# Kernel optimization log

Measured on AMD Instinct MI355X. Metric: run time of the kernel, lower is better.

## Reference

```python
import jax, jax.numpy as jnp
import numpy as np

N_NODES = 10000
N_EDGES = 160000
IN_FEATS = 512
HEADS = 8
OUT_FEATS = 64
NEG_SLOPE = 0.2


def setup_inputs() -> dict:
    key = jax.random.key(0)
    k_feat, k_w, k_al, k_ar, k_src, k_dst = jax.random.split(key, 6)
    feat = jax.random.normal(k_feat, (N_NODES, IN_FEATS), dtype=jnp.float32)
    # fc weight stored as [in_feats, heads*out_feats] (x @ W == Linear without bias)
    W = jax.random.normal(k_w, (IN_FEATS, HEADS * OUT_FEATS), dtype=jnp.float32) * 0.05
    attn_l = jax.random.normal(k_al, (HEADS, OUT_FEATS), dtype=jnp.float32) * 0.1
    attn_r = jax.random.normal(k_ar, (HEADS, OUT_FEATS), dtype=jnp.float32) * 0.1
    bias = jnp.zeros((HEADS * OUT_FEATS,), dtype=jnp.float32)
    src = jax.random.randint(k_src, (N_EDGES,), 0, N_NODES, dtype=jnp.int32)
    dst = jax.random.randint(k_dst, (N_EDGES,), 0, N_NODES, dtype=jnp.int32)
    return {"feat": feat, "W": W, "attn_l": attn_l, "attn_r": attn_r,
            "bias": bias, "src": src, "dst": dst}


def reference(feat, W, attn_l, attn_r, bias, src, dst):
    # 1) project features: [N, H, F]
    h = (feat @ W).reshape(N_NODES, HEADS, OUT_FEATS)
    # 2) per-node attention logits: el_i = a_l . h_i, er_j = a_r . h_j  -> [N, H]
    el = jnp.einsum('nhf,hf->nh', h, attn_l)
    er = jnp.einsum('nhf,hf->nh', h, attn_r)
    # 3) edge scores: u_add_v + LeakyReLU  -> [E, H]
    e = el[src] + er[dst]
    e = jnp.where(e > 0, e, NEG_SLOPE * e)
    # 4) edge softmax over incoming edges of each destination node
    m = jax.ops.segment_max(e, dst, num_segments=N_NODES)  # [N, H]
    a = jnp.exp(e - m[dst])
    s = jax.ops.segment_sum(a, dst, num_segments=N_NODES)  # [N, H]
    a = a / s[dst]
    # 5) weighted scatter-sum aggregation: sum_j a_ij * h_j  -> [N, H, F]
    msg = h[src] * a[:, :, None]                           # [E, H, F]
    rst = jax.ops.segment_sum(msg, dst, num_segments=N_NODES)
    # 6) bias
    rst = rst + bias.reshape(1, HEADS, OUT_FEATS)
    return rst
```

## Files before the change

### kernel.cpp

```cpp
#include <hip/hip_runtime.h>
#include <math.h>

#define N_NODES 10000
#define N_EDGES 160000
#define IN_FEATS 512
#define HEADS 8
#define OUT_FEATS 64
#define HF 512
#define NEG_SLOPE 0.2f
#define M_PAD 10048

typedef float  f32x4  __attribute__((ext_vector_type(4)));
typedef __bf16 bf16x8 __attribute__((ext_vector_type(8)));
typedef short  s16x8  __attribute__((ext_vector_type(8)));

__device__ __forceinline__ unsigned short f2bf_rn(float x) {
    unsigned u = __float_as_uint(x);
    unsigned r = u + 0x7FFFu + ((u >> 16) & 1u);
    return (unsigned short)(r >> 16);
}

__device__ __forceinline__ void gl_lds16(const void* g, void* l) {
    __builtin_amdgcn_global_load_lds((const __attribute__((address_space(1))) void*)g,
                                     (__attribute__((address_space(3))) void*)l, 16, 0, 0);
}

#define SF_BLOCKS 5024
#define PW_BLOCKS 64
#define HIST_BLOCKS 625
__global__ __launch_bounds__(256) void prep_kernel(const float* __restrict__ feat,
                                                   const float* __restrict__ W,
                                                   const int* __restrict__ dst,
                                                   unsigned short* __restrict__ Abf,
                                                   unsigned short* __restrict__ Bt,
                                                   int* __restrict__ counts) {
    __shared__ float tile[64][65];
    const int bid = blockIdx.x;
    const int tid = threadIdx.x;

    if (bid < SF_BLOCKS) {
        const int idx = bid * 256 + tid;
        const int row = idx >> 7;
        const int c4  = idx & 127;
        float4 v = make_float4(0.f, 0.f, 0.f, 0.f);
        if (row < N_NODES)
            v = *reinterpret_cast<const float4*>(feat + (size_t)row * IN_FEATS + c4 * 4);
        ushort4 o;
        o.x = f2bf_rn(v.x);
        o.y = f2bf_rn(v.y);
        o.z = f2bf_rn(v.z);
        o.w = f2bf_rn(v.w);
        *reinterpret_cast<ushort4*>(Abf + (size_t)row * IN_FEATS + c4 * 4) = o;
    } else if (bid < SF_BLOCKS + PW_BLOCKS) {
        const int b2 = bid - SF_BLOCKS;
        const int k0 = (b2 & 7) * 64;
        const int n0 = (b2 >> 3) * 64;
        #pragma unroll
        for (int i = 0; i < 4; ++i) {
            int f = tid + 256 * i;
            int r = f >> 4, c4 = f & 15;
            float4 v = *reinterpret_cast<const float4*>(W + (size_t)(k0 + r) * HF + n0 + c4 * 4);
            tile[r][c4 * 4 + 0] = v.x;
            tile[r][c4 * 4 + 1] = v.y;
            tile[r][c4 * 4 + 2] = v.z;
            tile[r][c4 * 4 + 3] = v.w;
        }
        __syncthreads();
        #pragma unroll
        for (int i = 0; i < 4; ++i) {
            int f = tid + 256 * i;
            int rn = f >> 4, c4 = f & 15;
            ushort4 o;
            o.x = f2bf_rn(tile[c4 * 4 + 0][rn]);
            o.y = f2bf_rn(tile[c4 * 4 + 1][rn]);
            o.z = f2bf_rn(tile[c4 * 4 + 2][rn]);
            o.w = f2bf_rn(tile[c4 * 4 + 3][rn]);
            *reinterpret_cast<ushort4*>(Bt + (size_t)(n0 + rn) * IN_FEATS + k0 + c4 * 4) = o;
        }
    } else {
        const int e = (bid - SF_BLOCKS - PW_BLOCKS) * 256 + tid;
        if (e < N_EDGES) atomicAdd(&counts[dst[e]], 1);
    }
}

#define GTM 64
#define GTN 128
#define GBK 32
__global__ __launch_bounds__(256) void gemm_mfma(const unsigned short* __restrict__ Abf,
                                                 const unsigned short* __restrict__ Bt,
                                                 const float* __restrict__ attn_l,
                                                 const float* __restrict__ attn_r,
                                                 unsigned short* __restrict__ hbf,
                                                 float* __restrict__ el,
                                                 float* __restrict__ er) {
    __shared__ unsigned short sA[2][GTM * GBK];
    __shared__ unsigned short sB[2][GTN * GBK];

    const int tid  = threadIdx.x;
    const int lane = tid & 63;
    const int w    = tid >> 6;
    const int wm   = w >> 1, wn = w & 1;
    const int m16  = lane & 15, quad = lane >> 4;
    const int row0 = blockIdx.y * GTM;
    const int col0 = blockIdx.x * GTN;
    const int hh   = blockIdx.x * 2 + wn;

    const int srow  = lane >> 2;
    const int kperm = ((lane & 3) ^ ((lane >> 4) & 3)) * 8;

    f32x4 acc[2][4] = {};

    auto stage = [&](int nb, int k0) {
        #pragma unroll
        for (int jj = 0; jj < 3; ++jj) {
            const int j = w * 3 + jj;
            if (j < 4) {
                const unsigned short* g = Abf
                    + (size_t)(row0 + j * 16 + srow) * IN_FEATS + k0 + kperm;
                gl_lds16(g, &sA[nb][j * 512]);
            } else {
                const int ch = j - 4;
                const unsigned short* g = Bt
                    + (size_t)(col0 + ch * 16 + srow) * IN_FEATS + k0 + kperm;
                gl_lds16(g, &sB[nb][ch * 512]);
            }
        }
    };

    stage(0, 0);
    int nb = 0;
    const int asw = (quad ^ ((m16 >> 2) & 3)) * 8;

    for (int kt = 0; kt < 16; ++kt) {
        __syncthreads();
        if (kt < 15) stage(nb ^ 1, (kt + 1) * GBK);

        s16x8 fa[2], fb[4];
        #pragma unroll
        for (int mi = 0; mi < 2; ++mi)
            fa[mi] = *reinterpret_cast<const s16x8*>(&sA[nb][(wm * 2 + mi) * 512 + m16 * 32 + asw]);
        #pragma unroll
        for (int ni = 0; ni < 4; ++ni)
            fb[ni] = *reinterpret_cast<const s16x8*>(&sB[nb][(wn * 4 + ni) * 512 + m16 * 32 + asw]);
        #pragma unroll
        for (int mi = 0; mi < 2; ++mi)
            #pragma unroll
            for (int ni = 0; ni < 4; ++ni)
                acc[mi][ni] = __builtin_amdgcn_mfma_f32_16x16x32_bf16(
                    __builtin_bit_cast(bf16x8, fa[mi]), __builtin_bit_cast(bf16x8, fb[ni]),
                    acc[mi][ni], 0, 0, 0);
        nb ^= 1;
    }

    float alw[4], arw[4];
    #pragma unroll
    for (int ni = 0; ni < 4; ++ni) {
        alw[ni] = attn_l[hh * OUT_FEATS + ni * 16 + m16];
        arw[ni] = attn_r[hh * OUT_FEATS + ni * 16 + m16];
    }
    #pragma unroll
    for (int mi = 0; mi < 2; ++mi) {
        #pragma unroll
        for (int r = 0; r < 4; ++r) {
            const int row = row0 + wm * 32 + mi * 16 + quad * 4 + r;
            if (row < N_NODES) {
                float pl = 0.f, pr = 0.f;
                #pragma unroll
                for (int ni = 0; ni < 4; ++ni) {
                    const float v = acc[mi][ni][r];
                    hbf[(size_t)row * HF + hh * OUT_FEATS + ni * 16 + m16] = f2bf_rn(v);
                    pl = fmaf(v, alw[ni], pl);
                    pr = fmaf(v, arw[ni], pr);
                }
                #pragma unroll
                for (int off = 1; off < 16; off <<= 1) {
                    pl += __shfl_xor(pl, off);
                    pr += __shfl_xor(pr, off);
                }
                if (m16 == 0) {
                    el[row * HEADS + hh] = pl;
                    er[row * HEADS + hh] = pr;
                }
            }
        }
    }
}

__global__ __launch_bounds__(1024) void scan_fast(const int* __restrict__ counts,
                                                  int* __restrict__ row_ptr,
                                                  int* __restrict__ cursor) {
    const int t = threadIdx.x;
    const int lane = t & 63, wid = t >> 6;
    for (int i = t; i < N_NODES; i += 1024) cursor[i] = 0;
    int loc[10];
    int tot = 0;
    #pragma unroll
    for (int j = 0; j < 10; ++j) {
        int idx = t * 10 + j;
        int c = (idx < N_NODES) ? counts[idx] : 0;
        loc[j] = tot;
        tot += c;
    }
    int inc = tot;
    #pragma unroll
    for (int off = 1; off < 64; off <<= 1) {
        int nb = __shfl_up(inc, off);
        if (lane >= off) inc += nb;
    }
    __shared__ int wbase[16];
    if (lane == 63) wbase[wid] = inc;
    __syncthreads();
    if (t == 0) {
        int r = 0;
        #pragma unroll
        for (int i = 0; i < 16; ++i) { int x = wbase[i]; wbase[i] = r; r += x; }
    }
    __syncthreads();
    const int base = wbase[wid] + inc - tot;
    #pragma unroll
    for (int j = 0; j < 10; ++j) {
        int idx = t * 10 + j;
        if (idx < N_NODES) row_ptr[idx] = base + loc[j];
    }
    if (t == 1023) row_ptr[N_NODES] = base + tot;
}

__global__ __launch_bounds__(256) void scatter_alpha(const int* __restrict__ src,
                                                     const int* __restrict__ dst,
                                                     const int* __restrict__ row_ptr,
                                                     int* __restrict__ cursor,
                                                     const float* __restrict__ el,
                                                     const float* __restrict__ er,
                                                     int* __restrict__ ssrc,
                                                     float* __restrict__ palpha) {
    const int e = blockIdx.x * 256 + threadIdx.x;
    if (e >= N_EDGES) return;
    const int d  = dst[e];
    const int sn = src[e];
    const int pos = row_ptr[d] + atomicAdd(&cursor[d], 1);
    ssrc[pos] = sn;

    float4 l0 = *reinterpret_cast<const float4*>(el + sn * 8);
    float4 l1 = *reinterpret_cast<const float4*>(el + sn * 8 + 4);
    float4 r0 = *reinterpret_cast<const float4*>(er + d * 8);
    float4 r1 = *reinterpret_cast<const float4*>(er + d * 8 + 4);
    float x[8] = {l0.x + r0.x, l0.y + r0.y, l0.z + r0.z, l0.w + r0.w,
                  l1.x + r1.x, l1.y + r1.y, l1.z + r1.z, l1.w + r1.w};
    float p[8];
    #pragma unroll
    for (int h = 0; h < 8; ++h) {
        float v = x[h] > 0.f ? x[h] : NEG_SLOPE * x[h];
        p[h] = __expf(v);
    }
    *reinterpret_cast<float4*>(palpha + (size_t)pos * 8)     = make_float4(p[0], p[1], p[2], p[3]);
    *reinterpret_cast<float4*>(palpha + (size_t)pos * 8 + 4) = make_float4(p[4], p[5], p[6], p[7]);
}

__global__ __launch_bounds__(256) void aggregate_kernel(const unsigned short* __restrict__ hbf,
                                                        const float* __restrict__ palpha,
                                                        const float* __restrict__ bias,
                                                        const int* __restrict__ row_ptr,
                                                        const int* __restrict__ ssrc,
                                                        float* __restrict__ out) {
    const int n    = (blockIdx.x * 256 + threadIdx.x) >> 6;
    const int lane = threadIdx.x & 63;
    if (n >= N_NODES) return;
    const int head = lane >> 3;
    const int beg = row_ptr[n];
    const int deg = row_ptr[n + 1] - beg;

    float4 b0 = *reinterpret_cast<const float4*>(bias + lane * 8);
    float4 b1 = *reinterpret_cast<const float4*>(bias + lane * 8 + 4);
    float* op = out + (size_t)n * HF + lane * 8;
    if (deg == 0) {
        *reinterpret_cast<float4*>(op)     = b0;
        *reinterpret_cast<float4*>(op + 4) = b1;
        return;
    }

    const int*   __restrict__ sp = ssrc + beg;
    const float* __restrict__ ap = palpha + (size_t)beg * 8 + head;
    const unsigned short* __restrict__ hb = hbf + lane * 8;

    float acc[8] = {};
    float s = 0.f;

    for (int k = 0; k < deg; k += 8) {
        float a[8]; int sx[8];
        #pragma unroll
        for (int j = 0; j < 8; ++j) {
            const int kk = k + j;
            const int kc = (kk < deg) ? kk : 0;
            sx[j] = sp[kc];
            a[j]  = (kk < deg) ? ap[(size_t)kc * 8] : 0.f;
        }
        uint4 u[8];
        #pragma unroll
        for (int j = 0; j < 8; ++j)
            u[j] = *reinterpret_cast<const uint4*>(hb + (size_t)sx[j] * HF);
        #pragma unroll
        for (int j = 0; j < 8; ++j) {
            const unsigned* wp = (const unsigned*)&u[j];
            s += a[j];
            #pragma unroll
            for (int q = 0; q < 4; ++q) {
                acc[2 * q]     = fmaf(a[j], __uint_as_float(wp[q] << 16),         acc[2 * q]);
                acc[2 * q + 1] = fmaf(a[j], __uint_as_float(wp[q] & 0xFFFF0000u), acc[2 * q + 1]);
            }
        }
    }

    const float inv = 1.0f / s;
    float4 o0 = make_float4(acc[0] * inv + b0.x, acc[1] * inv + b0.y,
                            acc[2] * inv + b0.z, acc[3] * inv + b0.w);
    float4 o1 = make_float4(acc[4] * inv + b1.x, acc[5] * inv + b1.y,
                            acc[6] * inv + b1.z, acc[7] * inv + b1.w);
    *reinterpret_cast<float4*>(op)     = o0;
    *reinterpret_cast<float4*>(op + 4) = o1;
}

extern "C" void kernel_launch(void* const* d_in, const int* in_sizes, int n_in,
                              void* d_out, int out_size, void* d_ws, size_t ws_size,
                              hipStream_t stream) {
    const float* feat   = (const float*)d_in[0];
    const float* W      = (const float*)d_in[1];
    const float* attn_l = (const float*)d_in[2];
    const float* attn_r = (const float*)d_in[3];
    const float* bias   = (const float*)d_in[4];
    const int*   src    = (const int*)d_in[5];
    const int*   dst    = (const int*)d_in[6];
    float* out = (float*)d_out;

    char* ws = (char*)d_ws;
    unsigned short* Abf    = (unsigned short*)ws; ws += (size_t)M_PAD * IN_FEATS * 2;
    unsigned short* Bt     = (unsigned short*)ws; ws += (size_t)IN_FEATS * HF * 2;
    unsigned short* hbf    = (unsigned short*)ws; ws += (size_t)N_NODES * HF * 2;
    float*          el_buf = (float*)ws;          ws += (size_t)N_NODES * HEADS * 4;
    float*          er_buf = (float*)ws;          ws += (size_t)N_NODES * HEADS * 4;
    float*          palpha = (float*)ws;          ws += (size_t)N_EDGES * HEADS * 4;
    int*            ssrc   = (int*)ws;            ws += (size_t)N_EDGES * 4;
    int*            counts = (int*)ws;            ws += (size_t)N_NODES * 4;
    int*            cursor = (int*)ws;            ws += (size_t)N_NODES * 4;
    int*            row_ptr= (int*)ws;            ws += (size_t)(N_NODES + 1) * 4;

    hipMemsetAsync(counts, 0, (size_t)N_NODES * 4, stream);

    prep_kernel<<<SF_BLOCKS + PW_BLOCKS + HIST_BLOCKS, 256, 0, stream>>>(
        feat, W, dst, Abf, Bt, counts);

    dim3 ggrid(HF / GTN, M_PAD / GTM);
    gemm_mfma<<<ggrid, 256, 0, stream>>>(Abf, Bt, attn_l, attn_r, hbf, el_buf, er_buf);

    scan_fast<<<1, 1024, 0, stream>>>(counts, row_ptr, cursor);

    scatter_alpha<<<(N_EDGES + 255) / 256, 256, 0, stream>>>(
        src, dst, row_ptr, cursor, el_buf, er_buf, ssrc, palpha);

    aggregate_kernel<<<(N_NODES * 64 + 255) / 256, 256, 0, stream>>>(
        hbf, palpha, bias, row_ptr, ssrc, out);
}
```

Measured before the change: 155.5 us.

## Fold scan into GEMM launch and restructure GEMM to full-K register A tiles

Moves the prefix-scan over in-degree counts into block 0 of the GEMM kernel, which removes one kernel launch. The GEMM is rewritten so each block computes a 64-row by one-head (64-column) tile. It loads the full K=512 slice of B into 64KB of swizzled LDS in a single pass and keeps each wave's A rows in registers for the whole K range, replacing the double-buffered K loop. This drops the per-iteration barriers, but the larger LDS footprint and register use lower occupancy. The scan now runs on 256 threads instead of 1024, which lengthens that block.

```diff
diff --git a/kernel.cpp b/kernel.cpp
--- a/kernel.cpp
+++ b/kernel.cpp
@@ -84,72 +84,95 @@
 }
 
 #define GTM 64
-#define GTN 128
-#define GBK 32
 __global__ __launch_bounds__(256) void gemm_mfma(const unsigned short* __restrict__ Abf,
                                                  const unsigned short* __restrict__ Bt,
                                                  const float* __restrict__ attn_l,
                                                  const float* __restrict__ attn_r,
                                                  unsigned short* __restrict__ hbf,
                                                  float* __restrict__ el,
-                                                 float* __restrict__ er) {
-    __shared__ unsigned short sA[2][GTM * GBK];
-    __shared__ unsigned short sB[2][GTN * GBK];
+                                                 float* __restrict__ er,
+                                                 const int* __restrict__ counts,
+                                                 int* __restrict__ row_ptr,
+                                                 int* __restrict__ cursor) {
+    __shared__ unsigned short sB[64 * 512];
 
     const int tid  = threadIdx.x;
+
+    if (blockIdx.x == 0) {
+        int* wb = (int*)sB;
+        const int lane = tid & 63, wid = tid >> 6;
+        for (int i = tid; i < N_NODES; i += 256) cursor[i] = 0;
+        int loc[40];
+        int tot = 0;
+        #pragma unroll
+        for (int j = 0; j < 40; ++j) {
+            int idx = tid * 40 + j;
+            int c = (idx < N_NODES) ? counts[idx] : 0;
+            loc[j] = tot;
+            tot += c;
+        }
+        int inc = tot;
+        #pragma unroll
+        for (int off = 1; off < 64; off <<= 1) {
+            int nb = __shfl_up(inc, off);
+            if (lane >= off) inc += nb;
+        }
+        if (lane == 63) wb[wid] = inc;
+        __syncthreads();
+        if (tid == 0) {
+            int r = 0;
+            #pragma unroll
+            for (int i = 0; i < 4; ++i) { int x = wb[i]; wb[i] = r; r += x; }
+        }
+        __syncthreads();
+        const int base = wb[wid] + inc - tot;
+        #pragma unroll
+        for (int j = 0; j < 40; ++j) {
+            int idx = tid * 40 + j;
+            if (idx < N_NODES) row_ptr[idx] = base + loc[j];
+        }
+        if (tid == 255) row_ptr[N_NODES] = base + tot;
+        return;
+    }
+
+    const int b    = blockIdx.x - 1;
+    const int hh   = b & 7;
+    const int row0 = (b >> 3) * GTM;
     const int lane = tid & 63;
     const int w    = tid >> 6;
-    const int wm   = w >> 1, wn = w & 1;
     const int m16  = lane & 15, quad = lane >> 4;
-    const int row0 = blockIdx.y * GTM;
-    const int col0 = blockIdx.x * GTN;
-    const int hh   = blockIdx.x * 2 + wn;
-
-    const int srow  = lane >> 2;
-    const int kperm = ((lane & 3) ^ ((lane >> 4) & 3)) * 8;
-
-    f32x4 acc[2][4] = {};
-
-    auto stage = [&](int nb, int k0) {
-        #pragma unroll
-        for (int jj = 0; jj < 3; ++jj) {
-            const int j = w * 3 + jj;
-            if (j < 4) {
-                const unsigned short* g = Abf
-                    + (size_t)(row0 + j * 16 + srow) * IN_FEATS + k0 + kperm;
-                gl_lds16(g, &sA[nb][j * 512]);
-            } else {
-                const int ch = j - 4;
-                const unsigned short* g = Bt
-                    + (size_t)(col0 + ch * 16 + srow) * IN_FEATS + k0 + kperm;
-                gl_lds16(g, &sB[nb][ch * 512]);
-            }
-        }
-    };
-
-    stage(0, 0);
-    int nb = 0;
-    const int asw = (quad ^ ((m16 >> 2) & 3)) * 8;
-
+    const int col0 = hh * 64;
+
+    const int arow = row0 + w * 16 + m16;
+    const unsigned short* ab = Abf + (size_t)arow * IN_FEATS + quad * 8;
+    s16x8 fa[16];
+    #pragma unroll
+    for (int kt = 0; kt < 16; ++kt)
+        fa[kt] = *reinterpret_cast<const s16x8*>(ab + kt * 32);
+
+    #pragma unroll
+    for (int it = 0; it < 16; ++it) {
+        const int c = w * 16 + it;
+        const int u = lane ^ (c & 7);
+        gl_lds16(Bt + (size_t)(col0 + c) * IN_FEATS + u * 8, sB + c * 512);
+    }
+    __syncthreads();
+
+    f32x4 acc[4] = {};
+    #pragma unroll
     for (int kt = 0; kt < 16; ++kt) {
-        __syncthreads();
-        if (kt < 15) stage(nb ^ 1, (kt + 1) * GBK);
-
-        s16x8 fa[2], fb[4];
-        #pragma unroll
-        for (int mi = 0; mi < 2; ++mi)
-            fa[mi] = *reinterpret_cast<const s16x8*>(&sA[nb][(wm * 2 + mi) * 512 + m16 * 32 + asw]);
+        s16x8 fb[4];
+        #pragma unroll
+        for (int ni = 0; ni < 4; ++ni) {
+            const int c = ni * 16 + m16;
+            const int v = (kt * 4 + quad) ^ (c & 7);
+            fb[ni] = *reinterpret_cast<const s16x8*>(sB + c * 512 + v * 8);
+        }
         #pragma unroll
         for (int ni = 0; ni < 4; ++ni)
-            fb[ni] = *reinterpret_cast<const s16x8*>(&sB[nb][(wn * 4 + ni) * 512 + m16 * 32 + asw]);
-        #pragma unroll
-        for (int mi = 0; mi < 2; ++mi)
-            #pragma unroll
-            for (int ni = 0; ni < 4; ++ni)
-                acc[mi][ni] = __builtin_amdgcn_mfma_f32_16x16x32_bf16(
-                    __builtin_bit_cast(bf16x8, fa[mi]), __builtin_bit_cast(bf16x8, fb[ni]),
-                    acc[mi][ni], 0, 0, 0);
-        nb ^= 1;
+            acc[ni] = __builtin_amdgcn_mfma_f32_16x16x32_bf16(
+                __builtin_bit_cast(bf16x8, fa[kt]), __builtin_bit_cast(bf16x8, fb[ni]),
+                acc[ni], 0, 0, 0);
     }
 
     float alw[4], arw[4];
@@ -159,70 +182,28 @@
         arw[ni] = attn_r[hh * OUT_FEATS + ni * 16 + m16];
     }
     #pragma unroll
-    for (int mi = 0; mi < 2; ++mi) {
-        #pragma unroll
-        for (int r = 0; r < 4; ++r) {
-            const int row = row0 + wm * 32 + mi * 16 + quad * 4 + r;
-            if (row < N_NODES) {
-                float pl = 0.f, pr = 0.f;
-                #pragma unroll
-                for (int ni = 0; ni < 4; ++ni) {
-                    const float v = acc[mi][ni][r];
-                    hbf[(size_t)row * HF + hh * OUT_FEATS + ni * 16 + m16] = f2bf_rn(v);
-                    pl = fmaf(v, alw[ni], pl);
-                    pr = fmaf(v, arw[ni], pr);
-                }
-                #pragma unroll
-                for (int off = 1; off < 16; off <<= 1) {
-                    pl += __shfl_xor(pl, off);
-                    pr += __shfl_xor(pr, off);
-                }
-                if (m16 == 0) {
-                    el[row * HEADS + hh] = pl;
-                    er[row * HEADS + hh] = pr;
-                }
+    for (int r = 0; r < 4; ++r) {
+        const int row = row0 + w * 16 + quad * 4 + r;
+        if (row < N_NODES) {
+            float pl = 0.f, pr = 0.f;
+            #pragma unroll
+            for (int ni = 0; ni < 4; ++ni) {
+                const float v = acc[ni][r];
+                hbf[(size_t)row * HF + hh * OUT_FEATS + ni * 16 + m16] = f2bf_rn(v);
+                pl = fmaf(v, alw[ni], pl);
+                pr = fmaf(v, arw[ni], pr);
             }
-        }
-    }
-}
-
-__global__ __launch_bounds__(1024) void scan_fast(const int* __restrict__ counts,
-                                                  int* __restrict__ row_ptr,
-                                                  int* __restrict__ cursor) {
-    const int t = threadIdx.x;
-    const int lane = t & 63, wid = t >> 6;
-    for (int i = t; i < N_NODES; i += 1024) cursor[i] = 0;
-    int loc[10];
-    int tot = 0;
-    #pragma unroll
-    for (int j = 0; j < 10; ++j) {
-        int idx = t * 10 + j;
-        int c = (idx < N_NODES) ? counts[idx] : 0;
-        loc[j] = tot;
-        tot += c;
-    }
-    int inc = tot;
-    #pragma unroll
-    for (int off = 1; off < 64; off <<= 1) {
-        int nb = __shfl_up(inc, off);
-        if (lane >= off) inc += nb;
-    }
-    __shared__ int wbase[16];
-    if (lane == 63) wbase[wid] = inc;
-    __syncthreads();
-    if (t == 0) {
-        int r = 0;
-        #pragma unroll
-        for (int i = 0; i < 16; ++i) { int x = wbase[i]; wbase[i] = r; r += x; }
-    }
-    __syncthreads();
-    const int base = wbase[wid] + inc - tot;
-    #pragma unroll
-    for (int j = 0; j < 10; ++j) {
-        int idx = t * 10 + j;
-        if (idx < N_NODES) row_ptr[idx] = base + loc[j];
-    }
-    if (t == 1023) row_ptr[N_NODES] = base + tot;
+            #pragma unroll
+            for (int off = 1; off < 16; off <<= 1) {
+                pl += __shfl_xor(pl, off);
+                pr += __shfl_xor(pr, off);
+            }
+            if (m16 == 0) {
+                el[row * HEADS + hh] = pl;
+                er[row * HEADS + hh] = pr;
+            }
+        }
+    }
 }
 
 __global__ __launch_bounds__(256) void scatter_alpha(const int* __restrict__ src,
@@ -348,10 +329,8 @@
     prep_kernel<<<SF_BLOCKS + PW_BLOCKS + HIST_BLOCKS, 256, 0, stream>>>(
         feat, W, dst, Abf, Bt, counts);
 
-    dim3 ggrid(HF / GTN, M_PAD / GTM);
-    gemm_mfma<<<ggrid, 256, 0, stream>>>(Abf, Bt, attn_l, attn_r, hbf, el_buf, er_buf);
-
-    scan_fast<<<1, 1024, 0, stream>>>(counts, row_ptr, cursor);
+    gemm_mfma<<<1 + 8 * (M_PAD / GTM), 256, 0, stream>>>(
+        Abf, Bt, attn_l, attn_r, hbf, el_buf, er_buf, counts, row_ptr, cursor);
 
     scatter_alpha<<<(N_EDGES + 255) / 256, 256, 0, stream>>>(
         src, dst, row_ptr, cursor, el_buf, er_buf, ssrc, palpha);
```

Result: no change. 157.5 us (+1.3%).
